# Kernel optimization log

Measured on AMD Instinct MI355X. Metric: run time of the kernel, lower is better.

The kernel has to match this reference:

```python
import jax, jax.numpy as jnp
import numpy as np

B, N, DIM = 4, 4096, 512
HEADS, DHEAD, CHUNK = 4, 128, 64
MAX_LR = 1.0
EPS = 1e-6


def rmsnorm(x):
    return x * jax.lax.rsqrt(jnp.mean(x * x, axis=-1, keepdims=True) + EPS)


def mem_mlp(params, x):
    # MemoryMLP depth=2: x @ W1 -> silu -> @ W2 (no biases)
    W1, W2 = params
    return jax.nn.silu(x @ W1) @ W2


def assoc_scan(gates, x):
    # linear recurrence y_i = g_i * y_{i-1} + x_i along axis=1 (chunks)
    def op(a, b):
        ga, xa = a
        gb, xb = b
        return (ga * gb, gb * xa + xb)
    _, y = jax.lax.associative_scan(op, (gates, x), axis=1)
    return y


def setup_inputs() -> dict:
    key = jax.random.key(0)
    ks = jax.random.split(key, 12)
    di = HEADS * DHEAD
    nrm = lambda k, shp, sc: jax.random.normal(k, shp, jnp.float32) * sc
    return {
        'seq': nrm(ks[0], (B, N, DIM), 1.0),
        'g_store': jnp.ones((DIM,), jnp.float32),
        'g_retrieve': jnp.ones((DIM,), jnp.float32),
        'W_q': nrm(ks[1], (DIM, di), DIM ** -0.5),
        'W_kv': nrm(ks[2], (DIM, 2 * di), DIM ** -0.5),
        'W_step': nrm(ks[3], (DIM, HEADS), DIM ** -0.5),
        'W_mom': nrm(ks[4], (DIM, HEADS), DIM ** -0.5),
        'W_decay': nrm(ks[5], (DIM, HEADS), DIM ** -0.5),
        'W_gate': nrm(ks[6], (DIM, HEADS), DIM ** -0.5),
        'gamma_mh': jnp.zeros((HEADS, 1, DHEAD), jnp.float32),
        'W_o': nrm(ks[7], (di, DIM), di ** -0.5),
        'M_W1': nrm(ks[8], (DHEAD, DHEAD), DHEAD ** -0.5),
        'M_W2': nrm(ks[9], (DHEAD, DHEAD), DHEAD ** -0.5),
    }


def reference(seq, g_store, g_retrieve, W_q, W_kv, W_step, W_mom, W_decay,
              W_gate, gamma_mh, W_o, M_W1, M_W2):
    b, n, dim = seq.shape
    h, d, c = HEADS, DHEAD, CHUNK
    nc = n // c
    bh = b * h

    # ---------------- store path ----------------
    s = rmsnorm(seq) * g_store                                   # (b,n,dim)
    lr = jax.nn.sigmoid(s @ W_step) * MAX_LR                     # (b,n,h)
    lr_c = lr.transpose(0, 2, 1).reshape(bh, nc, c)              # (bh,nc,c)
    chunked = s.reshape(b, nc, c, dim).mean(2)                   # (b,nc,dim)
    decay = jax.nn.sigmoid(chunked @ W_decay).transpose(0, 2, 1).reshape(bh, nc)
    mom = jax.nn.sigmoid(chunked @ W_mom).transpose(0, 2, 1).reshape(bh, nc)

    kv = s @ W_kv                                                # (b,n,2*h*d)
    k, v = jnp.split(kv, 2, axis=-1)
    to_chunks = lambda t: t.reshape(b, n, h, d).transpose(0, 2, 1, 3).reshape(bh, nc, c, d)
    k, v = to_chunks(k), to_chunks(v)

    # per-chunk gradient at the initial memory weights (vmap(grad))
    def chunk_loss(params, kc, lrc, vc):
        pred = mem_mlp(params, kc)                               # (c,d)
        loss = jnp.mean((pred - vc) ** 2, axis=-1)               # (c,)
        return jnp.sum(loss * lrc)

    gfn = jax.vmap(jax.vmap(jax.grad(chunk_loss),
                            in_axes=((None, None), 0, 0, 0)),
                   in_axes=((None, None), 0, 0, 0))
    g1, g2 = gfn((M_W1, M_W2), k, lr_c, v)                       # (bh,nc,d,d)
    s1, s2 = -g1, -g2                                            # surprises

    # momentum assoc scan: m_i = mom_i * m_{i-1} + s_i
    momg = mom[:, :, None, None]
    m1 = assoc_scan(momg, s1)
    m2 = assoc_scan(momg, s2)

    # decay-gated weight recurrence with prev = initial weights:
    # W_i = (1 - decay_i) * W_{i-1} + m_i,  W_0 = init
    def scan_with_init(gates, x, w0):
        g = jnp.concatenate([jnp.ones_like(gates[:, :1]), gates], axis=1)
        x0 = jnp.broadcast_to(w0, (bh, 1) + w0.shape)
        return assoc_scan(g, jnp.concatenate([x0, x], axis=1))   # (bh,nc+1,d,d)

    dg = (1.0 - decay)[:, :, None, None]
    u1 = scan_with_init(dg, m1, M_W1)
    u2 = scan_with_init(dg, m2, M_W2)
    # retrieval for chunk i uses weights after chunk i-1 (paper semantics)
    w1c, w2c = u1[:, :-1], u2[:, :-1]                            # (bh,nc,d,d)

    # ---------------- retrieve path ----------------
    r = rmsnorm(seq) * g_retrieve
    q = to_chunks(r @ W_q)                                       # (bh,nc,c,d)
    pred = jax.vmap(jax.vmap(lambda w1, w2, qc: mem_mlp((w1, w2), qc)))(w1c, w2c, q)
    out = pred.reshape(b, h, n, d)
    out = rmsnorm(out) * (gamma_mh + 1.0)                        # multihead rmsnorm
    gate = jax.nn.sigmoid(r @ W_gate)                            # (b,n,h)
    out = out * gate.transpose(0, 2, 1)[..., None]               # retrieve gate
    out = out.transpose(0, 2, 1, 3).reshape(b, n, h * d)         # merge heads
    return out @ W_o                                             # combine heads
```

## Files before the change

kernel.cpp:

```cpp
#include <hip/hip_runtime.h>

typedef unsigned short u16;
typedef unsigned int u32;
typedef __attribute__((ext_vector_type(8))) short s16x8;
typedef __attribute__((ext_vector_type(4))) float f32x4;

#define DEV __device__ __forceinline__
#define MFMA16(a,b,c) __builtin_amdgcn_mfma_f32_16x16x32_bf16(a,b,c,0,0,0)

DEV float bf2f(u16 x){ u32 u=((u32)x)<<16; float f; __builtin_memcpy(&f,&u,4); return f; }
DEV u16 f2bf(float f){ u32 u; __builtin_memcpy(&u,&f,4); u32 r=u+0x7FFFu+((u>>16)&1u); return (u16)(r>>16); }
DEV uint4 pack8(const float* f){
  uint4 v;
  v.x=(u32)f2bf(f[0])|((u32)f2bf(f[1])<<16);
  v.y=(u32)f2bf(f[2])|((u32)f2bf(f[3])<<16);
  v.z=(u32)f2bf(f[4])|((u32)f2bf(f[5])<<16);
  v.w=(u32)f2bf(f[6])|((u32)f2bf(f[7])<<16);
  return v;
}
DEV float sigm(float x){ return 1.0f/(1.0f+__expf(-x)); }

DEV void trans_tile_a(const float* src, u16* dst, int K, int Nn, int bx, int by,
                      int tid, bool act, float* ld )
{
  int n0 = bx*64, k0 = by*64;
  if (act){
    #pragma unroll
    for (int rr=0; rr<4; rr++){
      int kk = rr*16 + (tid>>4);
      int nn = (tid&15)*4;
      float4 v = *(const float4*)(src + (size_t)(k0+kk)*Nn + n0 + nn);
      ld[kk*65+nn]=v.x; ld[kk*65+nn+1]=v.y; ld[kk*65+nn+2]=v.z; ld[kk*65+nn+3]=v.w;
    }
  }
  __syncthreads();
  if (act){
    int nn2 = tid>>2, kb = (tid&3)*16;
    float o[16];
    #pragma unroll
    for (int j=0;j<16;j++) o[j] = ld[(kb+j)*65+nn2];
    u16* dp = dst + (size_t)(n0+nn2)*K + k0 + kb;
    *(uint4*)dp     = pack8(&o[0]);
    *(uint4*)(dp+8) = pack8(&o[8]);
  }
}

__global__ __launch_bounds__(512) void k_front(const float* __restrict__ seq,
    const float* __restrict__ gs, const float* __restrict__ gr,
    const float* __restrict__ Wstep, const float* __restrict__ Wgate,
    const float* __restrict__ Wdec, const float* __restrict__ Wmom,
    const float* __restrict__ Wkv, const float* __restrict__ Wq,
    const float* __restrict__ Wo, const float* __restrict__ MW1,
    const float* __restrict__ MW2,
    u16* __restrict__ s, u16* __restrict__ r,
    float* __restrict__ lr, float* __restrict__ gate,
    float* __restrict__ momv, float* __restrict__ dgv,
    u16* __restrict__ Wkvt, u16* __restrict__ Wqt, u16* __restrict__ Wot,
    u16* __restrict__ W1t, u16* __restrict__ W2t, u16* __restrict__ W2s)
{
  __shared__ float smem[8192];
  const int blk = blockIdx.x;
  const int tid = threadIdx.x;

  if (blk >= 256){
    int l = blk - 256;
    bool act = tid < 256;
    int t2 = tid & 255;
    if (l < 128)      trans_tile_a(Wkv, Wkvt, 512, 1024, l&15, l>>4, t2, act, smem);
    else if (l < 192){ int m = l-128; trans_tile_a(Wq, Wqt, 512, 512, m&7, m>>3, t2, act, smem); }
    else if (l < 256){ int m = l-192; trans_tile_a(Wo, Wot, 512, 512, m&7, m>>3, t2, act, smem); }
    else if (l < 260){ int m = l-256; trans_tile_a(MW1, W1t, 128, 128, m&1, m>>1, t2, act, smem); }
    else if (l < 264){ int m = l-260; trans_tile_a(MW2, W2t, 128, 128, m&1, m>>1, t2, act, smem); }
    else {
      __syncthreads();
      if (act){
        int e = ((l-264)*256 + t2)*8;
        float f[8];
        *(float4*)&f[0] = *(const float4*)(MW2+e);
        *(float4*)&f[4] = *(const float4*)(MW2+e+4);
        *(uint4*)(W2s+e) = pack8(f);
      }
    }
    return;
  }

  float* pchunk = smem;
  float* red    = smem + 4096;
  const int b = blk >> 6, ci = blk & 63;
  const int wv = tid >> 6, lane = tid & 63;
  const size_t rowbase = (size_t)b*4096 + (size_t)ci*64;

  float psum[8] = {0,0,0,0,0,0,0,0};
  #pragma unroll 1
  for (int tt=0; tt<8; tt++){
    int t = wv*8 + tt;
    const float* row = seq + (rowbase + t)*512;
    float x[8];
    *(float4*)&x[0] = *(const float4*)(row + lane*8);
    *(float4*)&x[4] = *(const float4*)(row + lane*8 + 4);
    float ss = 0.f;
    #pragma unroll
    for (int j=0;j<8;j++) ss += x[j]*x[j];
    #pragma unroll
    for (int o=32;o>=1;o>>=1) ss += __shfl_xor(ss, o, 64);
    float inv = rsqrtf(ss*(1.0f/512.0f) + 1e-6f);
    float al[4] = {0,0,0,0}, ag[4] = {0,0,0,0};
    float sv8[8], rv8[8];
    #pragma unroll
    for (int j=0;j<8;j++){
      int d = lane*8 + j;
      float sn = x[j]*inv;
      float sv = sn*gs[d];
      float rv = sn*gr[d];
      sv8[j]=sv; rv8[j]=rv;
      psum[j] += sv;
      float4 wst = *(const float4*)(Wstep + d*4);
      float4 wgt = *(const float4*)(Wgate + d*4);
      al[0]+=sv*wst.x; al[1]+=sv*wst.y; al[2]+=sv*wst.z; al[3]+=sv*wst.w;
      ag[0]+=rv*wgt.x; ag[1]+=rv*wgt.y; ag[2]+=rv*wgt.z; ag[3]+=rv*wgt.w;
    }
    *(uint4*)(s + (rowbase+t)*512 + lane*8) = pack8(sv8);
    *(uint4*)(r + (rowbase+t)*512 + lane*8) = pack8(rv8);
    #pragma unroll
    for (int o=32;o>=1;o>>=1){
      #pragma unroll
      for (int h=0;h<4;h++){ al[h] += __shfl_xor(al[h], o, 64); ag[h] += __shfl_xor(ag[h], o, 64); }
    }
    if (lane == 0){
      #pragma unroll
      for (int h=0;h<4;h++){
        lr[(rowbase+t)*4 + h]   = sigm(al[h]);
        gate[(rowbase+t)*4 + h] = sigm(ag[h]);
      }
    }
  }
  #pragma unroll
  for (int j=0;j<8;j++) pchunk[wv*512 + lane*8+j] = psum[j];
  __syncthreads();
  {
    int d = tid;
    float mean = 0.f;
    #pragma unroll
    for (int w=0;w<8;w++) mean += pchunk[w*512 + d];
    mean *= (1.0f/64.0f);
    #pragma unroll
    for (int h=0;h<4;h++){
      red[h*512 + d]     = mean*Wdec[d*4+h];
      red[(4+h)*512 + d] = mean*Wmom[d*4+h];
    }
  }
  __syncthreads();
  {
    float sum = 0.f;
    #pragma unroll
    for (int j=0;j<8;j++) sum += red[wv*512 + lane*8+j];
    #pragma unroll
    for (int o=32;o>=1;o>>=1) sum += __shfl_xor(sum, o, 64);
    if (lane == 0){
      if (wv < 4) dgv[((size_t)(b*4+wv))*64 + ci]      = 1.0f - sigm(sum);
      else        momv[((size_t)(b*4+(wv-4)))*64 + ci] = sigm(sum);
    }
  }
}

template<bool OUT_BF>
DEV void gemm_body(const u16* A, const u16* Bt, void* Cv, int K, int ldc,
                   int bx, int by, u16* sA, u16* sB)
{
  const int tid = threadIdx.x;
  const int wv = tid>>6, lane = tid&63, lrow = lane&15, lk = lane>>4;
  const int wm = (wv>>1)*64, wn = (wv&1)*64;
  const int rowbase = by*128, colbase = bx*128;
  const int srow = lane>>3;
  const int scol = (lane&7)*8;
  f32x4 acc[4][4] = {};
  for (int kc = 0; kc < K; kc += 64){
    __syncthreads();
    #pragma unroll
    for (int it=0; it<4; ++it){
      int seg = it*4 + wv;
      int row = seg*8 + srow;
      __builtin_amdgcn_global_load_lds(
        (const __attribute__((address_space(1))) void*)(A + (size_t)(rowbase+row)*K + kc + scol),
        (__attribute__((address_space(3))) void*)&sA[seg*512 + lane*8], 16, 0, 0);
      __builtin_amdgcn_global_load_lds(
        (const __attribute__((address_space(1))) void*)(Bt + (size_t)(colbase+row)*K + kc + scol),
        (__attribute__((address_space(3))) void*)&sB[seg*512 + lane*8], 16, 0, 0);
    }
    __syncthreads();
    #pragma unroll
    for (int k0=0;k0<2;k0++){
      s16x8 a[4], b[4];
      #pragma unroll
      for (int m=0;m<4;m++) a[m] = *(const s16x8*)&sA[(wm+m*16+lrow)*64 + k0*32 + lk*8];
      #pragma unroll
      for (int n=0;n<4;n++) b[n] = *(const s16x8*)&sB[(wn+n*16+lrow)*64 + k0*32 + lk*8];
      #pragma unroll
      for (int m=0;m<4;m++)
        #pragma unroll
        for (int n=0;n<4;n++)
          acc[m][n] = MFMA16(a[m], b[n], acc[m][n]);
    }
  }
  #pragma unroll
  for (int m=0;m<4;m++)
    #pragma unroll
    for (int n=0;n<4;n++)
      #pragma unroll
      for (int r=0;r<4;r++){
        int row = rowbase + wm + m*16 + lk*4 + r;
        int col = colbase + wn + n*16 + lrow;
        float v = acc[m][n][r];
        if (OUT_BF) ((u16*)Cv)[(size_t)row*ldc + col] = f2bf(v);
        else        ((float*)Cv)[(size_t)row*ldc + col] = v;
      }
}

__global__ __launch_bounds__(256) void k_gemmAB(const u16* __restrict__ A1,
    const u16* __restrict__ B1, u16* __restrict__ C1,
    const u16* __restrict__ A2, const u16* __restrict__ B2, u16* __restrict__ C2)
{
  __shared__ u16 sA[128*64];
  __shared__ u16 sB[128*64];
  int bid = blockIdx.x;
  if (bid < 1024){
    int s = (bid & 7)*128 + (bid >> 3);
    gemm_body<true>(A1, B1, C1, 512, 1024, s & 7, s >> 3, sA, sB);
  } else {
    int l = bid - 1024;
    int s = (l & 7)*64 + (l >> 3);
    gemm_body<true>(A2, B2, C2, 512, 512, s & 3, s >> 2, sA, sB);
  }
}

template<bool OUT_BF>
__global__ __launch_bounds__(256) void k_gemm1(const u16* __restrict__ A,
    const u16* __restrict__ Bt, void* __restrict__ Cv, int K, int ldc, int nbx, int cpx)
{
  __shared__ u16 sA[128*64];
  __shared__ u16 sB[128*64];
  int bid = blockIdx.x;
  int s = (bid & 7)*cpx + (bid >> 3);
  gemm_body<OUT_BF>(A, Bt, Cv, K, ldc, s % nbx, s / nbx, sA, sB);
}

__global__ __launch_bounds__(256,4) void k_grad(const u16* __restrict__ kv,
    const float* __restrict__ lr, const u16* __restrict__ W1t,
    const u16* __restrict__ W2t, const u16* __restrict__ W2s,
    u16* __restrict__ s1, u16* __restrict__ s2)
{
  __shared__ u16 bufR[64*136];
  __shared__ u16 bufAt[128*68];
  __shared__ u16 bufPt[128*68];
  __shared__ float lrs[64];

  const int blk = blockIdx.x;
  const int bhi = blk >> 6, ci = blk & 63;
  const int b = bhi >> 2, hd = bhi & 3;
  const int tid = threadIdx.x;
  const int wv = tid>>6, lane = tid&63, lrow = lane&15, lk = lane>>4;
  int col[2]; col[0] = wv*32 + lrow; col[1] = wv*32 + 16 + lrow;
  const size_t rowbase = (size_t)b*4096 + (size_t)ci*64;
  const u16* kvb = kv + rowbase*1024 + hd*128;

  #pragma unroll
  for (int rep=0;rep<4;rep++){
    int lin = rep*2048 + tid*8;
    int i = lin >> 7, d = lin & 127;
    *(uint4*)&bufR[i*136 + d] = *(const uint4*)(kvb + (size_t)i*1024 + d);
  }
  if (tid < 64) lrs[tid] = lr[(rowbase + tid)*4 + hd] * (2.0f/128.0f);
  __syncthreads();

  float spv[4][2][4];

  {
    f32x4 acc[4][2] = {};
    #pragma unroll
    for (int k0=0;k0<4;k0++){
      s16x8 w0 = *(const s16x8*)(W1t + col[0]*128 + k0*32 + lk*8);
      s16x8 w1 = *(const s16x8*)(W1t + col[1]*128 + k0*32 + lk*8);
      #pragma unroll
      for (int m=0;m<4;m++){
        s16x8 a = *(const s16x8*)&bufR[(m*16+lrow)*136 + k0*32 + lk*8];
        acc[m][0] = MFMA16(a, w0, acc[m][0]);
        acc[m][1] = MFMA16(a, w1, acc[m][1]);
      }
    }
    __syncthreads();
    #pragma unroll
    for (int m=0;m<4;m++)
      #pragma unroll
      for (int n=0;n<2;n++){
        int row0 = m*16 + lk*4;
        u16 av4[4];
        #pragma unroll
        for (int r=0;r<4;r++){
          float h = acc[m][n][r];
          float sg = sigm(h);
          av4[r] = f2bf(h*sg);
          spv[m][n][r] = sg*(1.0f + h*(1.0f - sg));
          bufR[(row0+r)*136 + col[n]] = av4[r];
        }
        *(uint2*)&bufAt[col[n]*68 + row0] = make_uint2(
          (u32)av4[0] | ((u32)av4[1]<<16), (u32)av4[2] | ((u32)av4[3]<<16));
      }
  }
  __syncthreads();

  {
    f32x4 acc[4][2] = {};
    #pragma unroll
    for (int k0=0;k0<4;k0++){
      s16x8 w0 = *(const s16x8*)(W2t + col[0]*128 + k0*32 + lk*8);
      s16x8 w1 = *(const s16x8*)(W2t + col[1]*128 + k0*32 + lk*8);
      #pragma unroll
      for (int m=0;m<4;m++){
        s16x8 a = *(const s16x8*)&bufR[(m*16+lrow)*136 + k0*32 + lk*8];
        acc[m][0] = MFMA16(a, w0, acc[m][0]);
        acc[m][1] = MFMA16(a, w1, acc[m][1]);
      }
    }
    u16 vv[4][2][4];
    #pragma unroll
    for (int m=0;m<4;m++)
      #pragma unroll
      for (int n=0;n<2;n++)
        #pragma unroll
        for (int r=0;r<4;r++)
          vv[m][n][r] = kvb[(size_t)(m*16+lk*4+r)*1024 + 512 + col[n]];
    __syncthreads();
    #pragma unroll
    for (int m=0;m<4;m++)
      #pragma unroll
      for (int n=0;n<2;n++){
        int row0 = m*16 + lk*4;
        u16 dp4[4];
        #pragma unroll
        for (int r=0;r<4;r++){
          float dp = lrs[row0+r]*(acc[m][n][r] - bf2f(vv[m][n][r]));
          dp4[r] = f2bf(dp);
          bufR[(row0+r)*136 + col[n]] = dp4[r];
        }
        *(uint2*)&bufPt[col[n]*68 + row0] = make_uint2(
          (u32)dp4[0] | ((u32)dp4[1]<<16), (u32)dp4[2] | ((u32)dp4[3]<<16));
      }
  }
  __syncthreads();

  {
    f32x4 da[4][2] = {};
    #pragma unroll
    for (int k0=0;k0<4;k0++){
      s16x8 w0 = *(const s16x8*)(W2s + col[0]*128 + k0*32 + lk*8);
      s16x8 w1 = *(const s16x8*)(W2s + col[1]*128 + k0*32 + lk*8);
      #pragma unroll
      for (int m=0;m<4;m++){
        s16x8 a = *(const s16x8*)&bufR[(m*16+lrow)*136 + k0*32 + lk*8];
        da[m][0] = MFMA16(a, w0, da[m][0]);
        da[m][1] = MFMA16(a, w1, da[m][1]);
      }
    }
    __syncthreads();
    #pragma unroll
    for (int m=0;m<4;m++)
      #pragma unroll
      for (int n=0;n<2;n++){
        int row0 = m*16 + lk*4;
        u16 dh4[4];
        #pragma unroll
        for (int r=0;r<4;r++) dh4[r] = f2bf(spv[m][n][r]*da[m][n][r]);
        *(uint2*)&bufR[col[n]*68 + row0] = make_uint2(
          (u32)dh4[0] | ((u32)dh4[1]<<16), (u32)dh4[2] | ((u32)dh4[3]<<16));
      }
  }

  const size_t outbase = (size_t)blk * 16384;

  s16x8 kbf[2][2];
  #pragma unroll
  for (int n=0;n<2;n++)
    #pragma unroll
    for (int k0=0;k0<2;k0++)
      #pragma unroll
      for (int j=0;j<8;j++)
        ((u16*)&kbf[n][k0])[j] = kvb[(size_t)(k0*32 + lk*8 + j)*1024 + col[n]];
  {
    f32x4 acc[8][2] = {};
    #pragma unroll
    for (int k0=0;k0<2;k0++){
      s16x8 bf0 = *(const s16x8*)&bufAt[col[0]*68 + k0*32 + lk*8];
      s16x8 bf1 = *(const s16x8*)&bufAt[col[1]*68 + k0*32 + lk*8];
      #pragma unroll
      for (int m=0;m<8;m++){
        s16x8 a = *(const s16x8*)&bufPt[(m*16+lrow)*68 + k0*32 + lk*8];
        acc[m][0] = MFMA16(a, bf0, acc[m][0]);
        acc[m][1] = MFMA16(a, bf1, acc[m][1]);
      }
    }
    #pragma unroll
    for (int m=0;m<8;m++)
      #pragma unroll
      for (int n=0;n<2;n++)
        #pragma unroll
        for (int r=0;r<4;r++)
          s2[outbase + (size_t)(m*16 + lk*4 + r)*128 + col[n]] = f2bf(-acc[m][n][r]);
  }
  __syncthreads();

  {
    f32x4 acc[8][2] = {};
    #pragma unroll
    for (int k0=0;k0<2;k0++)
      #pragma unroll
      for (int m=0;m<8;m++){
        s16x8 a = *(const s16x8*)&bufR[(m*16+lrow)*68 + k0*32 + lk*8];
        acc[m][0] = MFMA16(a, kbf[0][k0], acc[m][0]);
        acc[m][1] = MFMA16(a, kbf[1][k0], acc[m][1]);
      }
    #pragma unroll
    for (int m=0;m<8;m++)
      #pragma unroll
      for (int n=0;n<2;n++)
        #pragma unroll
        for (int r=0;r<4;r++)
          s1[outbase + (size_t)(m*16 + lk*4 + r)*128 + col[n]] = f2bf(-acc[m][n][r]);
  }
}

__global__ __launch_bounds__(256) void k_scan(const float* __restrict__ momv,
    const float* __restrict__ dgv, const float* __restrict__ MW1,
    const float* __restrict__ MW2, u16* __restrict__ s1w, u16* __restrict__ s2w)
{
  int bhi = blockIdx.x >> 5, eb = blockIdx.x & 31;
  int e0 = eb*512 + threadIdx.x*2;
  float u1a = MW1[(e0&127)*128 + (e0>>7)];
  float u1b = MW1[((e0+1)&127)*128 + ((e0+1)>>7)];
  float u2a = MW2[(e0&127)*128 + (e0>>7)];
  float u2b = MW2[((e0+1)&127)*128 + ((e0+1)>>7)];
  float m1a = 0.f, m1b = 0.f, m2a = 0.f, m2b = 0.f;
  size_t base = (size_t)bhi*64*16384 + e0;
  const float* mv = momv + bhi*64;
  const float* dv = dgv + bhi*64;
  #pragma unroll 4
  for (int t=0; t<64; t++){
    float g  = mv[t];
    float dg = dv[t];
    size_t idx = base + (size_t)t*16384;
    u32 a = *(const u32*)(s1w + idx);
    u32 c = *(const u32*)(s2w + idx);
    *(u32*)(s1w + idx) = (u32)f2bf(u1a) | ((u32)f2bf(u1b)<<16);
    *(u32*)(s2w + idx) = (u32)f2bf(u2a) | ((u32)f2bf(u2b)<<16);
    m1a = g*m1a + bf2f((u16)(a&0xffffu));
    m1b = g*m1b + bf2f((u16)(a>>16));
    m2a = g*m2a + bf2f((u16)(c&0xffffu));
    m2b = g*m2b + bf2f((u16)(c>>16));
    u1a = dg*u1a + m1a;
    u1b = dg*u1b + m1b;
    u2a = dg*u2a + m2a;
    u2b = dg*u2b + m2b;
  }
}

__global__ __launch_bounds__(512) void k_retr(const u16* __restrict__ qin,
    const u16* __restrict__ w1c, const u16* __restrict__ w2c,
    const float* __restrict__ gate, const float* __restrict__ gamma,
    u16* __restrict__ outp)
{
  __shared__ u16 bufA[64*132];
  __shared__ float rsum[8][64];
  const int blk = blockIdx.x;
  const int bhi = blk >> 6, ci = blk & 63;
  const int b = bhi >> 2, hd = bhi & 3;
  const int tid = threadIdx.x;
  const int wv = tid>>6, lane = tid&63, lrow = lane&15, lk = lane>>4;
  const int nb = wv*16;
  const int colw = nb + lrow;
  const size_t rowbase = (size_t)b*4096 + (size_t)ci*64;
  const u16* w1 = w1c + (size_t)blk*16384;
  const u16* w2 = w2c + (size_t)blk*16384;

  {
    s16x8 wf[4];
    #pragma unroll
    for (int k0=0;k0<4;k0++) wf[k0] = *(const s16x8*)(w1 + colw*128 + k0*32 + lk*8);
    f32x4 acc[4] = {};
    #pragma unroll
    for (int k0=0;k0<4;k0++){
      #pragma unroll
      for (int m=0;m<4;m++){
        s16x8 a = *(const s16x8*)(qin + (rowbase + m*16+lrow)*512 + hd*128 + k0*32 + lk*8);
        acc[m] = MFMA16(a, wf[k0], acc[m]);
      }
    }
    #pragma unroll
    for (int m=0;m<4;m++){
      #pragma unroll
      for (int r=0;r<4;r++){
        float h = acc[m][r];
        bufA[(m*16+lk*4+r)*132 + colw] = f2bf(h*sigm(h));
      }
    }
  }
  __syncthreads();

  f32x4 acc[4] = {};
  {
    s16x8 wf[4];
    #pragma unroll
    for (int k0=0;k0<4;k0++) wf[k0] = *(const s16x8*)(w2 + colw*128 + k0*32 + lk*8);
    #pragma unroll
    for (int k0=0;k0<4;k0++){
      #pragma unroll
      for (int m=0;m<4;m++){
        s16x8 a = *(const s16x8*)&bufA[(m*16+lrow)*132 + k0*32 + lk*8];
        acc[m] = MFMA16(a, wf[k0], acc[m]);
      }
    }
  }
  #pragma unroll
  for (int m=0;m<4;m++){
    #pragma unroll
    for (int r=0;r<4;r++){
      float p = acc[m][r]*acc[m][r];
      p += __shfl_xor(p, 1, 64);
      p += __shfl_xor(p, 2, 64);
      p += __shfl_xor(p, 4, 64);
      p += __shfl_xor(p, 8, 64);
      if (lrow == 0) rsum[wv][m*16 + lk*4 + r] = p;
    }
  }
  __syncthreads();
  float gm = gamma[hd*128 + colw] + 1.0f;
  #pragma unroll
  for (int m=0;m<4;m++){
    #pragma unroll
    for (int r=0;r<4;r++){
      int row = m*16 + lk*4 + r;
      float sum = rsum[0][row]+rsum[1][row]+rsum[2][row]+rsum[3][row]
                + rsum[4][row]+rsum[5][row]+rsum[6][row]+rsum[7][row];
      float inv = rsqrtf(sum*(1.0f/128.0f) + 1e-6f);
      float gt = gate[(rowbase+row)*4 + hd];
      outp[(rowbase+row)*512 + hd*128 + colw] = f2bf(acc[m][r]*inv*gm*gt);
    }
  }
}

extern "C" void kernel_launch(void* const* d_in, const int* in_sizes, int n_in,
                              void* d_out, int out_size, void* d_ws, size_t ws_size,
                              hipStream_t stream)
{
  const float* seq    = (const float*)d_in[0];
  const float* gstore = (const float*)d_in[1];
  const float* gret   = (const float*)d_in[2];
  const float* W_q    = (const float*)d_in[3];
  const float* W_kv   = (const float*)d_in[4];
  const float* W_step = (const float*)d_in[5];
  const float* W_mom  = (const float*)d_in[6];
  const float* W_dec  = (const float*)d_in[7];
  const float* W_gate = (const float*)d_in[8];
  const float* gamma  = (const float*)d_in[9];
  const float* W_o    = (const float*)d_in[10];
  const float* MW1    = (const float*)d_in[11];
  const float* MW2    = (const float*)d_in[12];
  float* out = (float*)d_out;

  const size_t NS = (size_t)16384*512;
  const size_t NG = (size_t)16*64*16384;
  size_t need = (5*NS + 2*NG + 524288 + 262144 + 262144 + 3*16384)*2
              + (2*65536 + 2048)*4;
  if (ws_size < need) return;

  char* ws = (char*)d_ws;
  u16* s_bf = (u16*)ws; ws += NS*2;
  u16* r_bf = (u16*)ws; ws += NS*2;
  u16* kv_bf= (u16*)ws; ws += 2*NS*2;
  u16* q_bf = (u16*)ws; ws += NS*2;
  u16* s1   = (u16*)ws; ws += NG*2;
  u16* s2   = (u16*)ws; ws += NG*2;
  u16* Wkvt = (u16*)ws; ws += (size_t)524288*2;
  u16* Wqt  = (u16*)ws; ws += (size_t)262144*2;
  u16* Wot  = (u16*)ws; ws += (size_t)262144*2;
  u16* W1tb = (u16*)ws; ws += (size_t)16384*2;
  u16* W2tb = (u16*)ws; ws += (size_t)16384*2;
  u16* W2sb = (u16*)ws; ws += (size_t)16384*2;
  float* lr   = (float*)ws; ws += (size_t)65536*4;
  float* gatep= (float*)ws; ws += (size_t)65536*4;
  float* momv = (float*)ws; ws += 1024*4;
  float* dgv  = (float*)ws; ws += 1024*4;
  u16* outp = s_bf;

  k_front<<<528, 512, 0, stream>>>(seq, gstore, gret, W_step, W_gate, W_dec, W_mom,
                                   W_kv, W_q, W_o, MW1, MW2,
                                   s_bf, r_bf, lr, gatep, momv, dgv,
                                   Wkvt, Wqt, Wot, W1tb, W2tb, W2sb);
  k_gemmAB<<<1536, 256, 0, stream>>>(s_bf, Wkvt, kv_bf, r_bf, Wqt, q_bf);
  k_grad<<<1024, 256, 0, stream>>>(kv_bf, lr, W1tb, W2tb, W2sb, s1, s2);
  k_scan<<<512, 256, 0, stream>>>(momv, dgv, MW1, MW2, s1, s2);
  k_retr<<<1024, 512, 0, stream>>>(q_bf, s1, s2, gatep, gamma, outp);
  k_gemm1<false><<<512, 256, 0, stream>>>(outp, Wot, out, 512, 512, 4, 64);
}
```

Before: 173.5 us.

## Store memory weights in MFMA fragment order and stage queries in LDS

The gradient kernel now writes s1/s2 in a fragment-swizzled layout that matches how the retrieval kernel loads MFMA B operands. Each lane can then read its weight fragment as a contiguous 16-byte chunk at lane*8 instead of a strided row gather. The scan kernel's initial-weight indexing is remapped to the same layout. The retrieval kernel also stages the query tile into shared memory once with coalesced loads, instead of every wave re-reading strided global rows, at the cost of extra LDS and a barrier.

```diff
diff --git a/kernel.cpp b/kernel.cpp
--- a/kernel.cpp
+++ b/kernel.cpp
@@ -19,6 +19,7 @@
   return v;
 }
 DEV float sigm(float x){ return 1.0f/(1.0f+__expf(-x)); }
+
 
 DEV void trans_tile_a(const float* src, u16* dst, int K, int Nn, int bx, int by,
                       int tid, bool act, float* ld )
@@ -260,6 +261,9 @@
   const int tid = threadIdx.x;
   const int wv = tid>>6, lane = tid&63, lrow = lane&15, lk = lane>>4;
   int col[2]; col[0] = wv*32 + lrow; col[1] = wv*32 + 16 + lrow;
+  const int f_hi[2] = { (lrow>>3)*128, ((16+lrow)>>3)*128 };
+  const int f_lo[2] = { lrow&7, (16+lrow)&7 };
+  const int fbase = wv*512;
   const size_t rowbase = (size_t)b*4096 + (size_t)ci*64;
   const u16* kvb = kv + rowbase*1024 + hd*128;
 
@@ -404,7 +408,7 @@
       for (int n=0;n<2;n++)
         #pragma unroll
         for (int r=0;r<4;r++)
-          s2[outbase + (size_t)(m*16 + lk*4 + r)*128 + col[n]] = f2bf(-acc[m][n][r]);
+          s2[outbase + m*2048 + fbase + f_hi[n] + (lk*4+r)*8 + f_lo[n]] = f2bf(-acc[m][n][r]);
   }
   __syncthreads();
 
@@ -424,7 +428,7 @@
       for (int n=0;n<2;n++)
         #pragma unroll
         for (int r=0;r<4;r++)
-          s1[outbase + (size_t)(m*16 + lk*4 + r)*128 + col[n]] = f2bf(-acc[m][n][r]);
+          s1[outbase + m*2048 + fbase + f_hi[n] + (lk*4+r)*8 + f_lo[n]] = f2bf(-acc[m][n][r]);
   }
 }
 
@@ -434,10 +438,12 @@
 {
   int bhi = blockIdx.x >> 5, eb = blockIdx.x & 31;
   int e0 = eb*512 + threadIdx.x*2;
-  float u1a = MW1[(e0&127)*128 + (e0>>7)];
-  float u1b = MW1[((e0+1)&127)*128 + ((e0+1)>>7)];
-  float u2a = MW2[(e0&127)*128 + (e0>>7)];
-  float u2b = MW2[((e0+1)&127)*128 + ((e0+1)>>7)];
+  int colD = ((e0>>11)<<4) + ((e0>>3)&15);
+  int kD   = ((e0>>9)&3)*32 + ((e0>>7)&3)*8 + (e0&7);
+  float u1a = MW1[kD*128 + colD];
+  float u1b = MW1[(kD+1)*128 + colD];
+  float u2a = MW2[kD*128 + colD];
+  float u2b = MW2[(kD+1)*128 + colD];
   float m1a = 0.f, m1b = 0.f, m2a = 0.f, m2b = 0.f;
   size_t base = (size_t)bhi*64*16384 + e0;
   const float* mv = momv + bhi*64;
@@ -467,6 +473,7 @@
     const float* __restrict__ gate, const float* __restrict__ gamma,
     u16* __restrict__ outp)
 {
+  __shared__ u16 bufQ[64*136];
   __shared__ u16 bufA[64*132];
   __shared__ float rsum[8][64];
   const int blk = blockIdx.x;
@@ -474,22 +481,30 @@
   const int b = bhi >> 2, hd = bhi & 3;
   const int tid = threadIdx.x;
   const int wv = tid>>6, lane = tid&63, lrow = lane&15, lk = lane>>4;
-  const int nb = wv*16;
-  const int colw = nb + lrow;
+  const int colw = wv*16 + lrow;
   const size_t rowbase = (size_t)b*4096 + (size_t)ci*64;
   const u16* w1 = w1c + (size_t)blk*16384;
   const u16* w2 = w2c + (size_t)blk*16384;
+  const int lane8 = lane*8;
+
+  #pragma unroll
+  for (int rep=0;rep<2;rep++){
+    int lin = rep*4096 + tid*8;
+    int i = lin>>7, d = lin&127;
+    *(uint4*)&bufQ[i*136 + d] = *(const uint4*)(qin + (rowbase+i)*512 + hd*128 + d);
+  }
+  __syncthreads();
 
   {
     s16x8 wf[4];
     #pragma unroll
-    for (int k0=0;k0<4;k0++) wf[k0] = *(const s16x8*)(w1 + colw*128 + k0*32 + lk*8);
+    for (int k0=0;k0<4;k0++) wf[k0] = *(const s16x8*)(w1 + wv*2048 + k0*512 + lane8);
     f32x4 acc[4] = {};
     #pragma unroll
     for (int k0=0;k0<4;k0++){
       #pragma unroll
       for (int m=0;m<4;m++){
-        s16x8 a = *(const s16x8*)(qin + (rowbase + m*16+lrow)*512 + hd*128 + k0*32 + lk*8);
+        s16x8 a = *(const s16x8*)&bufQ[(m*16+lrow)*136 + k0*32 + lk*8];
         acc[m] = MFMA16(a, wf[k0], acc[m]);
       }
     }
@@ -508,7 +523,7 @@
   {
     s16x8 wf[4];
     #pragma unroll
-    for (int k0=0;k0<4;k0++) wf[k0] = *(const s16x8*)(w2 + colw*128 + k0*32 + lk*8);
+    for (int k0=0;k0<4;k0++) wf[k0] = *(const s16x8*)(w2 + wv*2048 + k0*512 + lane8);
     #pragma unroll
     for (int k0=0;k0<4;k0++){
       #pragma unroll
```

Measured after the change: 171.5 us. No clear change (-1.2%).
